# Performance work log

Hardware: AMD Instinct MI355X
Metric: run time of the kernel (lower is better)

The kernel has to match this reference:

```python
import jax, jax.numpy as jnp
import numpy as np
from functools import partial

B, T_OUT, T_IN, L, D_IN, D_ATT = 8, 256, 512, 128, 128, 128


def setup_inputs() -> dict:
    key = jax.random.key(0)
    ks = jax.random.split(key, 8)
    s = 0.05  # small init scale for numerical stability
    return {
        "inputs": jax.random.normal(ks[0], (B, T_OUT, D_IN), jnp.float32),
        "attended_inputs": jax.random.normal(ks[1], (B, T_IN, D_ATT), jnp.float32),
        "lstm_kernel": jax.random.normal(ks[2], (D_IN, 4 * L), jnp.float32) * s,
        "lstm_rec_kernel": jax.random.normal(ks[3], (L, 4 * L), jnp.float32) * s,
        "lstm_bias": jnp.zeros((4 * L,), jnp.float32),
        "W1": jax.random.normal(ks[4], (D_ATT, L), jnp.float32) * s,
        "b1": jnp.zeros((L,), jnp.float32),
        "W2": jax.random.normal(ks[5], (L, L), jnp.float32) * s,
        "b2": jnp.zeros((L,), jnp.float32),
        "W3": jax.random.normal(ks[6], (L, 1), jnp.float32) * s,
        "b3": jnp.zeros((1,), jnp.float32),
    }


def _lstm(x, Wk, Wr, b):
    # x: (B, T, D_in). Keras gate order: i, f, c(g), o. Zero initial state.
    Bq = x.shape[0]
    h0 = jnp.zeros((Bq, L), x.dtype)
    c0 = jnp.zeros((Bq, L), x.dtype)
    xz = jnp.einsum('btd,dk->btk', x, Wk) + b  # precompute input projection

    def step(carry, zt):
        h, c = carry
        z = zt + h @ Wr
        i, f, g, o = jnp.split(z, 4, axis=-1)
        c_new = jax.nn.sigmoid(f) * c + jax.nn.sigmoid(i) * jnp.tanh(g)
        h_new = jax.nn.sigmoid(o) * jnp.tanh(c_new)
        return (h_new, c_new), h_new

    (h_T, c_T), hs = jax.lax.scan(step, (h0, c0), jnp.swapaxes(xz, 0, 1))
    return jnp.swapaxes(hs, 0, 1), h_T, c_T  # (B, T, L), (B, L), (B, L)


def reference(inputs, attended_inputs, lstm_kernel, lstm_rec_kernel, lstm_bias,
              W1, b1, W2, b2, W3, b3):
    # setup_attended: keys = dense1(attended_inputs)
    keys = attended_inputs @ W1 + b1  # (B, T_in, L)
    x, h, c = _lstm(inputs, lstm_kernel, lstm_rec_kernel, lstm_bias)  # (B, T_out, L)
    q = x @ W2 + b2  # (B, T_out, L)
    # Bahdanau additive score: tanh(keys[:,None] + q[:,:,None]) . W3 -> (B, T_out, T_in)
    t = jnp.tanh(keys[:, None, :, :] + q[:, :, None, :])  # (B, T_out, T_in, L)
    scores = jnp.einsum('bqkl,l->bqk', t, W3[:, 0]) + b3[0]
    attn = jax.nn.softmax(scores, axis=-1)
    weighted = jnp.einsum('bqk,bkd->bqd', attn, attended_inputs)  # (B, T_out, D_att)
    out = jnp.concatenate([x, weighted], axis=2)  # (B, T_out, L + D_att)
    return out, h, c
```

## Files before the change

kernel.cpp:

```cpp
#include <hip/hip_runtime.h>
#include <hip/hip_bf16.h>

#define XZ_OFF   1048576
#define KEYS_OFF 2097152
#define X_OFF    2621440
#define OUT_H    524288
#define OUT_C    525312

#define LDS_BARRIER() __asm__ __volatile__("s_waitcnt lgkmcnt(0)\n\ts_barrier" ::: "memory")

typedef _Float16 f16x8 __attribute__((ext_vector_type(8)));
typedef float fx4 __attribute__((ext_vector_type(4)));

__device__ __forceinline__ float fast_rcp(float x) { return __builtin_amdgcn_rcpf(x); }
__device__ __forceinline__ float fast_sig(float v) { return fast_rcp(1.f + __expf(-v)); }
__device__ __forceinline__ float fast_tanh(float v) { return 2.f * fast_rcp(1.f + __expf(-2.f * v)) - 1.f; }

__global__ __launch_bounds__(256)
void xz_prologue(const float* __restrict__ inp, const float* __restrict__ Wk,
                 const float* __restrict__ bias, float* __restrict__ ws) {
  _Float16* xz16 = (_Float16*)(ws + XZ_OFF);
  __shared__ float ar[8][128];
  const int tid = threadIdx.x;
  const int row0 = blockIdx.x * 8;
  for (int i = tid; i < 8 * 128; i += 256) ar[i >> 7][i & 127] = inp[row0 * 128 + i];
  __syncthreads();
  float acc[8][2];
  const float bb0 = bias[tid], bb1 = bias[tid + 256];
#pragma unroll
  for (int r = 0; r < 8; ++r) { acc[r][0] = bb0; acc[r][1] = bb1; }
  for (int d = 0; d < 128; d += 4) {
    float w0a = Wk[(d + 0) * 512 + tid], w0b = Wk[(d + 0) * 512 + tid + 256];
    float w1a = Wk[(d + 1) * 512 + tid], w1b = Wk[(d + 1) * 512 + tid + 256];
    float w2a = Wk[(d + 2) * 512 + tid], w2b = Wk[(d + 2) * 512 + tid + 256];
    float w3a = Wk[(d + 3) * 512 + tid], w3b = Wk[(d + 3) * 512 + tid + 256];
#pragma unroll
    for (int r = 0; r < 8; ++r) {
      float4 a4 = *(const float4*)&ar[r][d];
      acc[r][0] += a4.x * w0a + a4.y * w1a + a4.z * w2a + a4.w * w3a;
      acc[r][1] += a4.x * w0b + a4.y * w1b + a4.z * w2b + a4.w * w3b;
    }
  }
  const int u = tid & 127, g0 = tid >> 7;
#pragma unroll
  for (int r = 0; r < 8; ++r) {
    const int row = row0 + r, b = row >> 8, t = row & 255;
    const int base = ((t * 8 + b) * 128 + u) * 4;
    xz16[base + g0]     = (_Float16)acc[r][0];
    xz16[base + g0 + 2] = (_Float16)acc[r][1];
  }
}

__global__ __launch_bounds__(512, 1)
void lstm_scan(const float* __restrict__ Wrf, const float* __restrict__ att,
               const float* __restrict__ W1, const float* __restrict__ b1,
               const float* __restrict__ ws, float* __restrict__ out) {
  __shared__ _Float16 hb[2][552];
  __shared__ float ar[16][128];
  const int tid = threadIdx.x;

  if (blockIdx.x >= 2) {
    float* keys = (float*)ws + KEYS_OFF;
    const int row0 = (blockIdx.x - 2) * 16;
    for (int i = tid; i < 16 * 128; i += 512) ar[i >> 7][i & 127] = att[row0 * 128 + i];
    __syncthreads();
    const int l = tid & 127, r0 = tid >> 7;
    float acc[4];
    const float bl = b1[l];
#pragma unroll
    for (int i = 0; i < 4; ++i) acc[i] = bl;
    for (int d = 0; d < 128; d += 4) {
      float w0 = W1[(d + 0) * 128 + l], w1 = W1[(d + 1) * 128 + l];
      float w2 = W1[(d + 2) * 128 + l], w3 = W1[(d + 3) * 128 + l];
#pragma unroll
      for (int i = 0; i < 4; ++i) {
        float4 a4 = *(const float4*)&ar[r0 + 4 * i][d];
        acc[i] += a4.x * w0 + a4.y * w1 + a4.z * w2 + a4.w * w3;
      }
    }
#pragma unroll
    for (int i = 0; i < 4; ++i) keys[(row0 + r0 + 4 * i) * 128 + l] = acc[i];
    return;
  }

  const _Float16* xz16 = (const _Float16*)(ws + XZ_OFF);
  _Float16* x16 = (_Float16*)((float*)ws + X_OFF);
  const int b_base = blockIdx.x * 4;
  const int w = tid >> 6, lane = tid & 63;
  const int q = lane >> 4, p = lane & 15;
  const int b = p & 3, isel = p >> 2;
  const int u = 16 * w + 4 * isel + q;
  const int bg = b_base + b;

  f16x8 afr[4][4];
#pragma unroll
  for (int i = 0; i < 4; ++i) {
    const int col = (p & 3) * 128 + 16 * w + 4 * i + (p >> 2);
#pragma unroll
    for (int kt = 0; kt < 4; ++kt)
#pragma unroll
      for (int j = 0; j < 8; ++j)
        afr[i][kt][j] = (_Float16)Wrf[(kt * 32 + q * 8 + j) * 512 + col];
  }

  {
    _Float16* hp = &hb[0][0];
    for (int i = tid; i < 2 * 552; i += 512) hp[i] = (_Float16)0.f;
  }
  const fx4 zeroC = {0.f, 0.f, 0.f, 0.f};
  float cst = 0.f, hval = 0.f;
  const _Float16* xp = xz16 + (bg * 128 + u) * 4;
  uint2 pf0 = *(const uint2*)(xp);
  uint2 pf1 = *(const uint2*)(xp + 4096);
  uint2 pf2 = *(const uint2*)(xp + 8192);
  __syncthreads();

  const int brow = (p & 3) * 136;
  for (int t = 0; t < 256; ++t) {
    const _Float16* hrow = &hb[t & 1][brow];
    f16x8 bfr[4];
#pragma unroll
    for (int kt = 0; kt < 4; ++kt)
      bfr[kt] = *(const f16x8*)&hrow[kt * 32 + q * 8];
    fx4 acc[4];
#pragma unroll
    for (int i = 0; i < 4; ++i)
      acc[i] = __builtin_amdgcn_mfma_f32_16x16x32_f16(afr[i][0], bfr[0], zeroC, 0, 0, 0);
#pragma unroll
    for (int kt = 1; kt < 4; ++kt)
#pragma unroll
      for (int i = 0; i < 4; ++i)
        acc[i] = __builtin_amdgcn_mfma_f32_16x16x32_f16(afr[i][kt], bfr[kt], acc[i], 0, 0, 0);

    float z[4];
#pragma unroll
    for (int r = 0; r < 4; ++r) {
      float s01 = (isel & 1) ? acc[1][r] : acc[0][r];
      float s23 = (isel & 1) ? acc[3][r] : acc[2][r];
      z[r] = (isel & 2) ? s23 : s01;
    }

    uint2 cur = pf0;
    pf0 = pf1; pf1 = pf2;
    const int t3 = (t + 3 < 256) ? t + 3 : 255;
    pf2 = *(const uint2*)(xp + t3 * 4096);

    const _Float16* cf = (const _Float16*)&cur;
    const float zi = z[0] + (float)cf[0];
    const float zf = z[1] + (float)cf[1];
    const float zg = z[2] + (float)cf[2];
    const float zo = z[3] + (float)cf[3];
    cst = fast_sig(zf) * cst + fast_sig(zi) * fast_tanh(zg);
    hval = fast_sig(zo) * fast_tanh(cst);
    hb[(t + 1) & 1][b * 136 + u] = (_Float16)hval;
    x16[(bg * 256 + t) * 128 + u] = (_Float16)hval;
    LDS_BARRIER();
  }
  out[OUT_H + bg * 128 + u] = hval;
  out[OUT_C + bg * 128 + u] = cst;
}

__global__ __launch_bounds__(256)
void attn_out_k(const float* __restrict__ att, const float* __restrict__ W2c,
                const float* __restrict__ b2c, const float* __restrict__ W3c,
                const float* __restrict__ b3c, const float* __restrict__ ws,
                float* __restrict__ out) {
  const float* keys = ws + KEYS_OFF;
  const _Float16* x16 = (const _Float16*)(ws + X_OFF);
  __shared__ float qp[4][128];
  __shared__ float xr[4][128];
  __shared__ float sc[4][512];
  __shared__ float kt[64][129];
  __shared__ float w3s[128];
  const int tid = threadIdx.x;
  const int b = blockIdx.x >> 6, q0 = (blockIdx.x & 63) * 4;
  const int l = tid & 127, r0 = tid >> 7;
  if (tid < 128) w3s[tid] = W3c[tid];
  for (int i = tid; i < 4 * 128; i += 256)
    xr[i >> 7][i & 127] = (float)x16[(b * 256 + q0) * 128 + i];
  __syncthreads();
  {
    float qa[2];
    const float bl = b2c[l];
    qa[0] = bl; qa[1] = bl;
    for (int d = 0; d < 128; d += 4) {
      float w0 = W2c[(d + 0) * 128 + l], w1 = W2c[(d + 1) * 128 + l];
      float w2v = W2c[(d + 2) * 128 + l], w3v = W2c[(d + 3) * 128 + l];
#pragma unroll
      for (int i = 0; i < 2; ++i) {
        float4 a4 = *(const float4*)&xr[r0 + 2 * i][d];
        qa[i] += a4.x * w0 + a4.y * w1 + a4.z * w2v + a4.w * w3v;
      }
    }
#pragma unroll
    for (int i = 0; i < 2; ++i) {
      int rr = r0 + 2 * i;
      qp[rr][l] = qa[i];
      out[(b * 256 + q0 + rr) * 256 + l] = xr[rr][l];
    }
  }
  const float b3v = b3c[0];
  for (int kt0 = 0; kt0 < 512; kt0 += 64) {
    __syncthreads();
    for (int i = tid; i < 64 * 128; i += 256)
      kt[i >> 7][i & 127] = keys[(b * 512 + kt0 + (i >> 7)) * 128 + (i & 127)];
    __syncthreads();
    {
      const int rr = tid >> 6, k = tid & 63;
      float acc = 0.f;
      for (int ll = 0; ll < 128; ll += 4) {
        float4 q4 = *(const float4*)&qp[rr][ll];
        float4 w4 = *(const float4*)&w3s[ll];
        acc += fast_tanh(kt[k][ll + 0] + q4.x) * w4.x
             + fast_tanh(kt[k][ll + 1] + q4.y) * w4.y
             + fast_tanh(kt[k][ll + 2] + q4.z) * w4.z
             + fast_tanh(kt[k][ll + 3] + q4.w) * w4.w;
      }
      sc[rr][kt0 + k] = acc + b3v;
    }
  }
  __syncthreads();
  {
    const int wave = tid >> 6, lane = tid & 63;
    float v[8];
#pragma unroll
    for (int i = 0; i < 8; ++i) v[i] = sc[wave][lane + i * 64];
    float m = v[0];
#pragma unroll
    for (int i = 1; i < 8; ++i) m = fmaxf(m, v[i]);
#pragma unroll
    for (int off = 32; off > 0; off >>= 1) m = fmaxf(m, __shfl_xor(m, off));
    float e[8], s = 0.f;
#pragma unroll
    for (int i = 0; i < 8; ++i) { e[i] = __expf(v[i] - m); s += e[i]; }
#pragma unroll
    for (int off = 32; off > 0; off >>= 1) s += __shfl_xor(s, off);
    const float inv = fast_rcp(s);
#pragma unroll
    for (int i = 0; i < 8; ++i) sc[wave][lane + i * 64] = e[i] * inv;
  }
  __syncthreads();
  {
    const float* attb = att + b * 512 * 128;
    float wa[2] = {0.f, 0.f};
    for (int k = 0; k < 512; k += 4) {
      float a0 = attb[(k + 0) * 128 + l];
      float a1 = attb[(k + 1) * 128 + l];
      float a2 = attb[(k + 2) * 128 + l];
      float a3 = attb[(k + 3) * 128 + l];
#pragma unroll
      for (int i = 0; i < 2; ++i) {
        float4 p4 = *(const float4*)&sc[r0 + 2 * i][k];
        wa[i] += p4.x * a0 + p4.y * a1 + p4.z * a2 + p4.w * a3;
      }
    }
#pragma unroll
    for (int i = 0; i < 2; ++i)
      out[(b * 256 + q0 + r0 + 2 * i) * 256 + 128 + l] = wa[i];
  }
}

extern "C" void kernel_launch(void* const* d_in, const int* in_sizes, int n_in,
                              void* d_out, int out_size, void* d_ws, size_t ws_size,
                              hipStream_t stream) {
  const float* inputs   = (const float*)d_in[0];
  const float* attended = (const float*)d_in[1];
  const float* Wk       = (const float*)d_in[2];
  const float* Wr       = (const float*)d_in[3];
  const float* bias     = (const float*)d_in[4];
  const float* W1       = (const float*)d_in[5];
  const float* b1       = (const float*)d_in[6];
  const float* W2       = (const float*)d_in[7];
  const float* b2       = (const float*)d_in[8];
  const float* W3       = (const float*)d_in[9];
  const float* b3       = (const float*)d_in[10];
  float* out = (float*)d_out;
  float* ws = (float*)d_ws;

  hipLaunchKernelGGL(xz_prologue, dim3(256), dim3(256), 0, stream, inputs, Wk, bias, ws);
  hipLaunchKernelGGL(lstm_scan, dim3(258), dim3(512), 0, stream,
                     Wr, attended, W1, b1, ws, out);
  hipLaunchKernelGGL(attn_out_k, dim3(512), dim3(256), 0, stream,
                     attended, W2, b2, W3, b3, ws, out);
}
```

Baseline: 307.7 us.

## Halve LSTM scan block to 4 waves with two hidden units per thread

The recurrent LSTM scan block drops from 8 waves to 4, and each thread now computes two hidden units, holding twice the recurrent-weight MFMA fragments in registers. Each wave issues 32 MFMAs per step instead of 16. The goal is to make the per-timestep barrier cheaper and cut cross-wave synchronisation on the serial critical path. The cost is a longer per-wave MFMA chain and gate computation each step, plus higher register pressure; the keys side-blocks adapt to 256 threads.

```diff
diff --git a/kernel.cpp b/kernel.cpp
--- a/kernel.cpp
+++ b/kernel.cpp
@@ -51,7 +51,7 @@
   }
 }
 
-__global__ __launch_bounds__(512, 1)
+__global__ __launch_bounds__(256, 1)
 void lstm_scan(const float* __restrict__ Wrf, const float* __restrict__ att,
                const float* __restrict__ W1, const float* __restrict__ b1,
                const float* __restrict__ ws, float* __restrict__ out) {
@@ -62,24 +62,24 @@
   if (blockIdx.x >= 2) {
     float* keys = (float*)ws + KEYS_OFF;
     const int row0 = (blockIdx.x - 2) * 16;
-    for (int i = tid; i < 16 * 128; i += 512) ar[i >> 7][i & 127] = att[row0 * 128 + i];
+    for (int i = tid; i < 16 * 128; i += 256) ar[i >> 7][i & 127] = att[row0 * 128 + i];
     __syncthreads();
     const int l = tid & 127, r0 = tid >> 7;
-    float acc[4];
+    float acc[8];
     const float bl = b1[l];
 #pragma unroll
-    for (int i = 0; i < 4; ++i) acc[i] = bl;
+    for (int i = 0; i < 8; ++i) acc[i] = bl;
     for (int d = 0; d < 128; d += 4) {
       float w0 = W1[(d + 0) * 128 + l], w1 = W1[(d + 1) * 128 + l];
       float w2 = W1[(d + 2) * 128 + l], w3 = W1[(d + 3) * 128 + l];
 #pragma unroll
-      for (int i = 0; i < 4; ++i) {
-        float4 a4 = *(const float4*)&ar[r0 + 4 * i][d];
+      for (int i = 0; i < 8; ++i) {
+        float4 a4 = *(const float4*)&ar[r0 + 2 * i][d];
         acc[i] += a4.x * w0 + a4.y * w1 + a4.z * w2 + a4.w * w3;
       }
     }
 #pragma unroll
-    for (int i = 0; i < 4; ++i) keys[(row0 + r0 + 4 * i) * 128 + l] = acc[i];
+    for (int i = 0; i < 8; ++i) keys[(row0 + r0 + 2 * i) * 128 + l] = acc[i];
     return;
   }
 
@@ -89,30 +89,36 @@
   const int w = tid >> 6, lane = tid & 63;
   const int q = lane >> 4, p = lane & 15;
   const int b = p & 3, isel = p >> 2;
-  const int u = 16 * w + 4 * isel + q;
+  const int u0 = 16 * w + 4 * isel + q;
+  const int u1 = 64 + u0;
   const int bg = b_base + b;
 
-  f16x8 afr[4][4];
-#pragma unroll
-  for (int i = 0; i < 4; ++i) {
-    const int col = (p & 3) * 128 + 16 * w + 4 * i + (p >> 2);
-#pragma unroll
-    for (int kt = 0; kt < 4; ++kt)
-#pragma unroll
-      for (int j = 0; j < 8; ++j)
-        afr[i][kt][j] = (_Float16)Wrf[(kt * 32 + q * 8 + j) * 512 + col];
+  f16x8 afr[2][4][4];
+#pragma unroll
+  for (int jj = 0; jj < 2; ++jj) {
+    const int base = 64 * jj + 16 * w;
+#pragma unroll
+    for (int i = 0; i < 4; ++i) {
+      const int col = (p & 3) * 128 + base + 4 * i + (p >> 2);
+#pragma unroll
+      for (int kt = 0; kt < 4; ++kt)
+#pragma unroll
+        for (int j = 0; j < 8; ++j)
+          afr[jj][i][kt][j] = (_Float16)Wrf[(kt * 32 + q * 8 + j) * 512 + col];
+    }
   }
 
   {
     _Float16* hp = &hb[0][0];
-    for (int i = tid; i < 2 * 552; i += 512) hp[i] = (_Float16)0.f;
+    for (int i = tid; i < 2 * 552; i += 256) hp[i] = (_Float16)0.f;
   }
   const fx4 zeroC = {0.f, 0.f, 0.f, 0.f};
-  float cst = 0.f, hval = 0.f;
-  const _Float16* xp = xz16 + (bg * 128 + u) * 4;
-  uint2 pf0 = *(const uint2*)(xp);
-  uint2 pf1 = *(const uint2*)(xp + 4096);
-  uint2 pf2 = *(const uint2*)(xp + 8192);
+  float cst0 = 0.f, cst1 = 0.f, hval0 = 0.f, hval1 = 0.f;
+  const _Float16* xp0 = xz16 + (bg * 128 + u0) * 4;
+  const _Float16* xp1 = xz16 + (bg * 128 + u1) * 4;
+  uint2 pa0 = *(const uint2*)(xp0),        pb0 = *(const uint2*)(xp1);
+  uint2 pa1 = *(const uint2*)(xp0 + 4096), pb1 = *(const uint2*)(xp1 + 4096);
+  uint2 pa2 = *(const uint2*)(xp0 + 8192), pb2 = *(const uint2*)(xp1 + 8192);
   __syncthreads();
 
   const int brow = (p & 3) * 136;
@@ -122,42 +128,59 @@
 #pragma unroll
     for (int kt = 0; kt < 4; ++kt)
       bfr[kt] = *(const f16x8*)&hrow[kt * 32 + q * 8];
-    fx4 acc[4];
-#pragma unroll
-    for (int i = 0; i < 4; ++i)
-      acc[i] = __builtin_amdgcn_mfma_f32_16x16x32_f16(afr[i][0], bfr[0], zeroC, 0, 0, 0);
+    fx4 acc[2][4];
+#pragma unroll
+    for (int jj = 0; jj < 2; ++jj)
+#pragma unroll
+      for (int i = 0; i < 4; ++i)
+        acc[jj][i] = __builtin_amdgcn_mfma_f32_16x16x32_f16(afr[jj][i][0], bfr[0], zeroC, 0, 0, 0);
 #pragma unroll
     for (int kt = 1; kt < 4; ++kt)
 #pragma unroll
-      for (int i = 0; i < 4; ++i)
-        acc[i] = __builtin_amdgcn_mfma_f32_16x16x32_f16(afr[i][kt], bfr[kt], acc[i], 0, 0, 0);
-
-    float z[4];
+      for (int jj = 0; jj < 2; ++jj)
+#pragma unroll
+        for (int i = 0; i < 4; ++i)
+          acc[jj][i] = __builtin_amdgcn_mfma_f32_16x16x32_f16(afr[jj][i][kt], bfr[kt], acc[jj][i], 0, 0, 0);
+
+    float z0[4], z1[4];
 #pragma unroll
     for (int r = 0; r < 4; ++r) {
-      float s01 = (isel & 1) ? acc[1][r] : acc[0][r];
-      float s23 = (isel & 1) ? acc[3][r] : acc[2][r];
-      z[r] = (isel & 2) ? s23 : s01;
-    }
-
-    uint2 cur = pf0;
-    pf0 = pf1; pf1 = pf2;
+      float s01 = (isel & 1) ? acc[0][1][r] : acc[0][0][r];
+      float s23 = (isel & 1) ? acc[0][3][r] : acc[0][2][r];
+      z0[r] = (isel & 2) ? s23 : s01;
+      float t01 = (isel & 1) ? acc[1][1][r] : acc[1][0][r];
+      float t23 = (isel & 1) ? acc[1][3][r] : acc[1][2][r];
+      z1[r] = (isel & 2) ? t23 : t01;
+    }
+
+    uint2 ca = pa0, cb = pb0;
+    pa0 = pa1; pa1 = pa2; pb0 = pb1; pb1 = pb2;
     const int t3 = (t + 3 < 256) ? t + 3 : 255;
-    pf2 = *(const uint2*)(xp + t3 * 4096);
-
-    const _Float16* cf = (const _Float16*)&cur;
-    const float zi = z[0] + (float)cf[0];
-    const float zf = z[1] + (float)cf[1];
-    const float zg = z[2] + (float)cf[2];
-    const float zo = z[3] + (float)cf[3];
-    cst = fast_sig(zf) * cst + fast_sig(zi) * fast_tanh(zg);
-    hval = fast_sig(zo) * fast_tanh(cst);
-    hb[(t + 1) & 1][b * 136 + u] = (_Float16)hval;
-    x16[(bg * 256 + t) * 128 + u] = (_Float16)hval;
+    pa2 = *(const uint2*)(xp0 + t3 * 4096);
+    pb2 = *(const uint2*)(xp1 + t3 * 4096);
+
+    const _Float16* cf0 = (const _Float16*)&ca;
+    const _Float16* cf1 = (const _Float16*)&cb;
+    const float zi0 = z0[0] + (float)cf0[0], zf0 = z0[1] + (float)cf0[1];
+    const float zg0 = z0[2] + (float)cf0[2], zo0 = z0[3] + (float)cf0[3];
+    const float zi1 = z1[0] + (float)cf1[0], zf1 = z1[1] + (float)cf1[1];
+    const float zg1 = z1[2] + (float)cf1[2], zo1 = z1[3] + (float)cf1[3];
+    cst0 = fast_sig(zf0) * cst0 + fast_sig(zi0) * fast_tanh(zg0);
+    cst1 = fast_sig(zf1) * cst1 + fast_sig(zi1) * fast_tanh(zg1);
+    hval0 = fast_sig(zo0) * fast_tanh(cst0);
+    hval1 = fast_sig(zo1) * fast_tanh(cst1);
+    _Float16* hnxt = &hb[(t + 1) & 1][b * 136];
+    hnxt[u0] = (_Float16)hval0;
+    hnxt[u1] = (_Float16)hval1;
+    _Float16* xo = x16 + (bg * 256 + t) * 128;
+    xo[u0] = (_Float16)hval0;
+    xo[u1] = (_Float16)hval1;
     LDS_BARRIER();
   }
-  out[OUT_H + bg * 128 + u] = hval;
-  out[OUT_C + bg * 128 + u] = cst;
+  out[OUT_H + bg * 128 + u0] = hval0;
+  out[OUT_H + bg * 128 + u1] = hval1;
+  out[OUT_C + bg * 128 + u0] = cst0;
+  out[OUT_C + bg * 128 + u1] = cst1;
 }
 
 __global__ __launch_bounds__(256)
@@ -278,7 +301,7 @@
   float* ws = (float*)d_ws;
 
   hipLaunchKernelGGL(xz_prologue, dim3(256), dim3(256), 0, stream, inputs, Wk, bias, ws);
-  hipLaunchKernelGGL(lstm_scan, dim3(258), dim3(512), 0, stream,
+  hipLaunchKernelGGL(lstm_scan, dim3(258), dim3(256), 0, stream,
                      Wr, attended, W1, b1, ws, out);
   hipLaunchKernelGGL(attn_out_k, dim3(512), dim3(256), 0, stream,
                      attended, W2, b2, W3, b3, ws, out);
```

Result: slower. 345.8 us (+12.4%).

## Fuse input-projection prologue into scan kernel with atomic-counter handoff

Applied to the files above, without the earlier changes.

Removes the separate xz_prologue launch. The 256 worker blocks of the scan kernel now compute the input projection first and then the attention keys. Each worker bumps a global atomic counter after writing its xz rows. The two scan blocks load their recurrent weight fragments and then spin on that counter before reading xz, which overlaps the prologue with scan setup and saves one launch. The counter is never reset: the target value assumes the workspace is pre-filled with the 0xAA byte pattern before every call. If that fill does not happen the kernel deadlocks or races, and the spin-wait assumes all 258 blocks are co-resident.

```diff
diff --git a/kernel.cpp b/kernel.cpp
--- a/kernel.cpp
+++ b/kernel.cpp
@@ -16,75 +16,74 @@
 __device__ __forceinline__ float fast_sig(float v) { return fast_rcp(1.f + __expf(-v)); }
 __device__ __forceinline__ float fast_tanh(float v) { return 2.f * fast_rcp(1.f + __expf(-2.f * v)) - 1.f; }
 
-__global__ __launch_bounds__(256)
-void xz_prologue(const float* __restrict__ inp, const float* __restrict__ Wk,
-                 const float* __restrict__ bias, float* __restrict__ ws) {
-  _Float16* xz16 = (_Float16*)(ws + XZ_OFF);
-  __shared__ float ar[8][128];
-  const int tid = threadIdx.x;
-  const int row0 = blockIdx.x * 8;
-  for (int i = tid; i < 8 * 128; i += 256) ar[i >> 7][i & 127] = inp[row0 * 128 + i];
-  __syncthreads();
-  float acc[8][2];
-  const float bb0 = bias[tid], bb1 = bias[tid + 256];
-#pragma unroll
-  for (int r = 0; r < 8; ++r) { acc[r][0] = bb0; acc[r][1] = bb1; }
-  for (int d = 0; d < 128; d += 4) {
-    float w0a = Wk[(d + 0) * 512 + tid], w0b = Wk[(d + 0) * 512 + tid + 256];
-    float w1a = Wk[(d + 1) * 512 + tid], w1b = Wk[(d + 1) * 512 + tid + 256];
-    float w2a = Wk[(d + 2) * 512 + tid], w2b = Wk[(d + 2) * 512 + tid + 256];
-    float w3a = Wk[(d + 3) * 512 + tid], w3b = Wk[(d + 3) * 512 + tid + 256];
-#pragma unroll
-    for (int r = 0; r < 8; ++r) {
-      float4 a4 = *(const float4*)&ar[r][d];
-      acc[r][0] += a4.x * w0a + a4.y * w1a + a4.z * w2a + a4.w * w3a;
-      acc[r][1] += a4.x * w0b + a4.y * w1b + a4.z * w2b + a4.w * w3b;
-    }
-  }
-  const int u = tid & 127, g0 = tid >> 7;
-#pragma unroll
-  for (int r = 0; r < 8; ++r) {
-    const int row = row0 + r, b = row >> 8, t = row & 255;
-    const int base = ((t * 8 + b) * 128 + u) * 4;
-    xz16[base + g0]     = (_Float16)acc[r][0];
-    xz16[base + g0 + 2] = (_Float16)acc[r][1];
-  }
-}
-
-__global__ __launch_bounds__(512, 1)
-void lstm_scan(const float* __restrict__ Wrf, const float* __restrict__ att,
-               const float* __restrict__ W1, const float* __restrict__ b1,
-               const float* __restrict__ ws, float* __restrict__ out) {
+__global__ __launch_bounds__(512)
+void main_k(const float* __restrict__ inp, const float* __restrict__ att,
+            const float* __restrict__ Wk, const float* __restrict__ bias,
+            const float* __restrict__ W1, const float* __restrict__ b1,
+            const float* __restrict__ Wrf, float* __restrict__ ws,
+            float* __restrict__ out) {
   __shared__ _Float16 hb[2][552];
   __shared__ float ar[16][128];
   const int tid = threadIdx.x;
+  int* cnt = (int*)ws;
+  const int target = (int)0xAAAAAAAA + 256;
 
   if (blockIdx.x >= 2) {
-    float* keys = (float*)ws + KEYS_OFF;
-    const int row0 = (blockIdx.x - 2) * 16;
-    for (int i = tid; i < 16 * 128; i += 512) ar[i >> 7][i & 127] = att[row0 * 128 + i];
-    __syncthreads();
-    const int l = tid & 127, r0 = tid >> 7;
-    float acc[4];
-    const float bl = b1[l];
-#pragma unroll
-    for (int i = 0; i < 4; ++i) acc[i] = bl;
-    for (int d = 0; d < 128; d += 4) {
-      float w0 = W1[(d + 0) * 128 + l], w1 = W1[(d + 1) * 128 + l];
-      float w2 = W1[(d + 2) * 128 + l], w3 = W1[(d + 3) * 128 + l];
-#pragma unroll
-      for (int i = 0; i < 4; ++i) {
-        float4 a4 = *(const float4*)&ar[r0 + 4 * i][d];
-        acc[i] += a4.x * w0 + a4.y * w1 + a4.z * w2 + a4.w * w3;
-      }
-    }
-#pragma unroll
-    for (int i = 0; i < 4; ++i) keys[(row0 + r0 + 4 * i) * 128 + l] = acc[i];
+    _Float16* xz16 = (_Float16*)(ws + XZ_OFF);
+    const int row0 = (blockIdx.x - 2) * 8;
+    for (int i = tid; i < 8 * 128; i += 512) ar[i >> 7][i & 127] = inp[row0 * 128 + i];
+    __syncthreads();
+    {
+      float acc[8];
+      const float bb = bias[tid];
+#pragma unroll
+      for (int r = 0; r < 8; ++r) acc[r] = bb;
+      for (int d = 0; d < 128; d += 4) {
+        float w0 = Wk[(d + 0) * 512 + tid], w1 = Wk[(d + 1) * 512 + tid];
+        float w2 = Wk[(d + 2) * 512 + tid], w3 = Wk[(d + 3) * 512 + tid];
+#pragma unroll
+        for (int r = 0; r < 8; ++r) {
+          float4 a4 = *(const float4*)&ar[r][d];
+          acc[r] += a4.x * w0 + a4.y * w1 + a4.z * w2 + a4.w * w3;
+        }
+      }
+      const int u = tid & 127, g = tid >> 7;
+#pragma unroll
+      for (int r = 0; r < 8; ++r) {
+        const int row = row0 + r, b = row >> 8, t = row & 255;
+        xz16[((t * 8 + b) * 128 + u) * 4 + g] = (_Float16)acc[r];
+      }
+    }
+    __syncthreads();
+    if (tid == 0)
+      __hip_atomic_fetch_add(cnt, 1, __ATOMIC_RELEASE, __HIP_MEMORY_SCOPE_AGENT);
+    {
+      float* keys = ws + KEYS_OFF;
+      const int row0k = (blockIdx.x - 2) * 16;
+      for (int i = tid; i < 16 * 128; i += 512) ar[i >> 7][i & 127] = att[row0k * 128 + i];
+      __syncthreads();
+      const int l = tid & 127, r0 = tid >> 7;
+      float acc[4];
+      const float bl = b1[l];
+#pragma unroll
+      for (int i = 0; i < 4; ++i) acc[i] = bl;
+      for (int d = 0; d < 128; d += 4) {
+        float w0 = W1[(d + 0) * 128 + l], w1 = W1[(d + 1) * 128 + l];
+        float w2 = W1[(d + 2) * 128 + l], w3 = W1[(d + 3) * 128 + l];
+#pragma unroll
+        for (int i = 0; i < 4; ++i) {
+          float4 a4 = *(const float4*)&ar[r0 + 4 * i][d];
+          acc[i] += a4.x * w0 + a4.y * w1 + a4.z * w2 + a4.w * w3;
+        }
+      }
+#pragma unroll
+      for (int i = 0; i < 4; ++i) keys[(row0k + r0 + 4 * i) * 128 + l] = acc[i];
+    }
     return;
   }
 
   const _Float16* xz16 = (const _Float16*)(ws + XZ_OFF);
-  _Float16* x16 = (_Float16*)((float*)ws + X_OFF);
+  _Float16* x16 = (_Float16*)(ws + X_OFF);
   const int b_base = blockIdx.x * 4;
   const int w = tid >> 6, lane = tid & 63;
   const int q = lane >> 4, p = lane & 15;
@@ -102,18 +101,22 @@
       for (int j = 0; j < 8; ++j)
         afr[i][kt][j] = (_Float16)Wrf[(kt * 32 + q * 8 + j) * 512 + col];
   }
-
   {
     _Float16* hp = &hb[0][0];
     for (int i = tid; i < 2 * 552; i += 512) hp[i] = (_Float16)0.f;
   }
+  if (tid == 0) {
+    while (__hip_atomic_load(cnt, __ATOMIC_ACQUIRE, __HIP_MEMORY_SCOPE_AGENT) != target)
+      __builtin_amdgcn_s_sleep(8);
+  }
+  __syncthreads();
+
   const fx4 zeroC = {0.f, 0.f, 0.f, 0.f};
   float cst = 0.f, hval = 0.f;
   const _Float16* xp = xz16 + (bg * 128 + u) * 4;
   uint2 pf0 = *(const uint2*)(xp);
   uint2 pf1 = *(const uint2*)(xp + 4096);
   uint2 pf2 = *(const uint2*)(xp + 8192);
-  __syncthreads();
 
   const int brow = (p & 3) * 136;
   for (int t = 0; t < 256; ++t) {
@@ -277,9 +280,8 @@
   float* out = (float*)d_out;
   float* ws = (float*)d_ws;
 
-  hipLaunchKernelGGL(xz_prologue, dim3(256), dim3(256), 0, stream, inputs, Wk, bias, ws);
-  hipLaunchKernelGGL(lstm_scan, dim3(258), dim3(512), 0, stream,
-                     Wr, attended, W1, b1, ws, out);
+  hipLaunchKernelGGL(main_k, dim3(258), dim3(512), 0, stream,
+                     inputs, attended, Wk, bias, W1, b1, Wr, ws, out);
   hipLaunchKernelGGL(attn_out_k, dim3(512), dim3(256), 0, stream,
                      attended, W2, b2, W3, b3, ws, out);
 }
```

Result: slower. 314.6 us (+2.2%).
